# Performance work log

Measured on AMD Instinct MI355X. Metric: run time of the kernel, lower is better.

## Reference

```python
import jax, jax.numpy as jnp
import numpy as np

N = 8000       # n_sample (nodes)
F = 128        # n_feature
H = 128        # n_hidden
E = 256000     # edges (avg degree 32)
NPOOL = 3
K = 10         # propagation steps (args.k)
NC = 2         # n_class
ALPHA = 0.0    # Propagation(alpha=0.0)
CENTS = [400, 20, 1]   # node_pool = round(N**(1/NPOOL)) = 20; n_cent = round(prev/20)


def setup_inputs():
    key = jax.random.key(0)
    ks = jax.random.split(key, 40)
    def nrm(i, shape, scale=1.0):
        return jax.random.normal(ks[i], shape, jnp.float32) * scale
    x = nrm(0, (N, F))
    x_cov = nrm(1, (N, F))
    edge_rows = jax.random.randint(ks[2], (E,), 0, N, dtype=jnp.int32)
    edge_cols = jax.random.randint(ks[3], (E,), 0, N, dtype=jnp.int32)
    adj_vals = jax.random.uniform(ks[4], (E,), jnp.float32)
    raw = jax.random.uniform(ks[5], (E,), jnp.float32) + 0.1
    deg = jax.ops.segment_sum(raw, edge_rows, num_segments=N)
    norm_vals = raw / deg[edge_rows]   # row-normalized adjacency values
    inp = dict(x=x, x_cov=x_cov, edge_rows=edge_rows, edge_cols=edge_cols,
               adj_vals=adj_vals, norm_vals=norm_vals,
               bn_gamma=jnp.ones((F,), jnp.float32), bn_beta=jnp.zeros((F,), jnp.float32))
    i = 6
    for p, nc in enumerate(CENTS):
        inp['c%d_W1' % p] = nrm(i, (F, H), F ** -0.5); i += 1
        inp['c%d_b1' % p] = jnp.zeros((H,), jnp.float32)
        inp['c%d_W2' % p] = nrm(i, (H, nc), H ** -0.5); i += 1
        inp['c%d_b2' % p] = jnp.zeros((nc,), jnp.float32)
    inp['mW1'] = nrm(i, (F, H), F ** -0.5); i += 1
    inp['mb1'] = jnp.zeros((H,), jnp.float32)
    inp['a1'] = jnp.full((1,), 0.25, jnp.float32)   # PReLU slope
    inp['mW2'] = nrm(i, (H, H), H ** -0.5); i += 1
    inp['mb2'] = jnp.zeros((H,), jnp.float32)
    inp['a2'] = jnp.full((1,), 0.25, jnp.float32)
    inp['mW3'] = nrm(i, (H, NC), H ** -0.5); i += 1
    inp['mb3'] = jnp.zeros((NC,), jnp.float32)
    return inp


def _node_corr(z):
    # per-node decomposition of torch.corrcoef(z.T).sum(1):
    #   _node_corr(z).sum(0) == corrcoef(z.T).sum(1)
    zc = z - z.mean(0, keepdims=True)
    zc = zc / (jnp.linalg.norm(zc, axis=0, keepdims=True) + 1e-12)
    return zc * zc.sum(1, keepdims=True)   # [n, F]


def reference(x, x_cov, edge_rows, edge_cols, adj_vals, norm_vals, bn_gamma, bn_beta,
              c0_W1, c0_b1, c0_W2, c0_b2, c1_W1, c1_b1, c1_W2, c1_b2,
              c2_W1, c2_b1, c2_W2, c2_b2, mW1, mb1, a1, mW2, mb2, a2, mW3, mb3):
    # BatchNorm1d (training statistics, biased variance, eps=1e-5)
    mu, var = x.mean(0), x.var(0)
    x = (x - mu) / jnp.sqrt(var + 1e-5) * bn_gamma + bn_beta
    x0 = x

    # --- multi-level clustering / pooling (ClusteringLayer) ---
    cl_params = [(c0_W1, c0_b1, c0_W2, c0_b2), (c1_W1, c1_b1, c1_W2, c1_b2),
                 (c2_W1, c2_b1, c2_W2, c2_b2)]
    masks, corrs = [], []
    xc = x_cov
    for W1, b1, W2, b2 in cl_params:
        h = jax.nn.relu(xc @ W1 + b1)
        S = jax.nn.softmax(h @ W2 + b2, axis=-1)        # soft assignment [n_prev, n_cent]
        corrs.append(_node_corr(xc))                     # corr at the input level
        masks.append(S)
        xc = (S.T @ xc) / (S.sum(0)[:, None] + 1e-12)    # pooled centroid features
    corrs.append(_node_corr(x).sum(0))   # == torch.corrcoef(x.T).sum(1), shape [F]

    # --- gains: sigmoid(corr_{i+1} - normalize_adj(mask_i).T @ corr_i) ---
    gains = []
    for i in range(NPOOL):
        rn = masks[i] / (masks[i].sum(1, keepdims=True) + 1e-12)  # row-normalized (symmetric=False)
        gains.append(jax.nn.sigmoid(corrs[i + 1] - rn.T @ corrs[i]))

    # --- per-feature diagonal-masked sparse matmul chains, restricted to adj's edge set ---
    # projector to original nodes: P_i = masks[0] @ ... @ masks[i]
    P = [masks[0]]
    for i in range(1, NPOOL - 1):
        P.append(P[-1] @ masks[i])
    # (M M^T)[r,c] with M = P_i @ diag(g[:,j]) evaluated only on adj edges, all features at once
    def edge_mask(Pi, g):
        return jnp.einsum('ek,ek,kf->ef', Pi[edge_rows], Pi[edge_cols], g * g)  # [E, F]
    ms = [edge_mask(P[i], gains[i]) for i in reversed(range(NPOOL - 1))]  # i = NPOOL-2 .. 0
    ms = jnp.stack(ms, axis=0).transpose(2, 0, 1)   # [F, NPOOL-1, E]

    def per_feature(a, m_steps):   # sequential carry of adj over feature loop (matches torch)
        def inner(ai, mrow):
            ai = ai * mrow          # adj = adj * mask (elementwise on edge values)
            return ai, ai
        a, temps = jax.lax.scan(inner, a, m_steps)
        return a, temps.sum(0)      # adjs[j] = torch.sparse.sum(stack(temp), dim=0)
    _, adjs = jax.lax.scan(per_feature, adj_vals, ms)   # [F, E] edge values

    # --- diffusion propagation: x <- (1-alpha) * norm_adj @ x + alpha * x0, k times ---
    for _ in range(K):
        agg = jax.ops.segment_sum(norm_vals[:, None] * x[edge_cols], edge_rows, num_segments=N)
        x = (1.0 - ALPHA) * agg + ALPHA * x0

    # --- 3-layer MLP with PReLU + log_softmax ---
    prelu = lambda z, a: jnp.where(z >= 0, z, a * z)
    h = prelu(x @ mW1 + mb1, a1)
    h = prelu(h @ mW2 + mb2, a2)
    logits = h @ mW3 + mb3
    return jax.nn.log_softmax(logits, axis=1), adjs
```

## Files before the change

### kernel.cpp

```cpp
#include <hip/hip_runtime.h>
#include <hip/hip_bf16.h>

typedef __hip_bfloat16 bf16;
typedef __attribute__((ext_vector_type(8))) short s16x8;
typedef __attribute__((ext_vector_type(4))) float f32x4;

static constexpr int NN = 8000;
static constexpr int FF = 128;
static constexpr int EE = 256000;
static constexpr int NC0 = 400;
static constexpr int NC1 = 20;

__device__ __forceinline__ float b2f(bf16 v) { return __bfloat162float(v); }
__device__ __forceinline__ bf16 f2b(float v) { return __float2bfloat16(v); }
__device__ __forceinline__ short f2bs(float v) {
    bf16 h = __float2bfloat16(v);
    return __builtin_bit_cast(short, h);
}
__device__ __forceinline__ float ldw(float v) { return v; }
__device__ __forceinline__ float ldw(bf16 v) { return __bfloat162float(v); }

template <int NW>
__device__ __forceinline__ float block_sum(float v, float* sb) {
    #pragma unroll
    for (int o = 32; o > 0; o >>= 1) v += __shfl_down(v, o, 64);
    int t = threadIdx.x;
    if ((t & 63) == 0) sb[t >> 6] = v;
    __syncthreads();
    float s = 0.f;
    #pragma unroll
    for (int i = 0; i < NW; ++i) s += sb[i];
    __syncthreads();
    return s;
}

template <int NW>
__device__ __forceinline__ float block_max(float v, float* sb) {
    #pragma unroll
    for (int o = 32; o > 0; o >>= 1) v = fmaxf(v, __shfl_down(v, o, 64));
    int t = threadIdx.x;
    if ((t & 63) == 0) sb[t >> 6] = v;
    __syncthreads();
    float m = sb[0];
    #pragma unroll
    for (int i = 1; i < NW; ++i) m = fmaxf(m, sb[i]);
    __syncthreads();
    return m;
}

__global__ void k_fill_b16(bf16* __restrict__ p, float v, long n) {
    long i = (long)blockIdx.x * 256 + threadIdx.x;
    long stride = (long)gridDim.x * 256;
    for (; i < n; i += stride) p[i] = f2b(v);
}

__global__ __launch_bounds__(256)
void k_tsplit(const float* __restrict__ src, bf16* __restrict__ dh, bf16* __restrict__ dl,
              bf16* __restrict__ sh, bf16* __restrict__ sl, int M, int N) {
    __shared__ float t[32][33];
    int bx = blockIdx.x * 32, by = blockIdx.y * 32;
    int x = threadIdx.x;
    for (int y = threadIdx.y; y < 32; y += 8) {
        int m = by + y, n = bx + x;
        if (m < M && n < N) {
            float v = src[(long)m * N + n];
            t[y][x] = v;
            if (sh) {
                bf16 h = f2b(v);
                sh[(long)m * N + n] = h;
                sl[(long)m * N + n] = f2b(v - b2f(h));
            }
        }
    }
    __syncthreads();
    for (int y = threadIdx.y; y < 32; y += 8) {
        int n = bx + y, m = by + x;
        if (n < N && m < M) {
            float v = t[x][y];
            bf16 h = f2b(v);
            dh[(long)n * M + m] = h;
            dl[(long)n * M + m] = f2b(v - b2f(h));
        }
    }
}

__global__ __launch_bounds__(256)
void k_cstat(const float* __restrict__ x, const float* __restrict__ xcov,
             float* __restrict__ acc4) {
    __shared__ float sb[4][256];
    int t = threadIdx.x;
    int col = t & 127, half = t >> 7;
    int rend = min(NN, (blockIdx.x + 1) * 80);
    float sx = 0.f, qx = 0.f, sc = 0.f, qc = 0.f;
    for (int r = blockIdx.x * 80 + half; r < rend; r += 2) {
        float v = x[(long)r * FF + col];
        sx += v; qx += v * v;
        float w = xcov[(long)r * FF + col];
        sc += w; qc += w * w;
    }
    sb[0][t] = sx; sb[1][t] = qx; sb[2][t] = sc; sb[3][t] = qc;
    __syncthreads();
    if (t < 128) {
        atomicAdd(&acc4[0 * 128 + col], sb[0][t] + sb[0][t + 128]);
        atomicAdd(&acc4[1 * 128 + col], sb[1][t] + sb[1][t + 128]);
        atomicAdd(&acc4[2 * 128 + col], sb[2][t] + sb[2][t + 128]);
        atomicAdd(&acc4[3 * 128 + col], sb[3][t] + sb[3][t + 128]);
    }
}

__global__ void k_cfin(const float* __restrict__ acc4, const float* __restrict__ gamma,
                       const float* __restrict__ beta, float* __restrict__ bnsc,
                       float* __restrict__ bnsh, float* __restrict__ statmu,
                       float* __restrict__ statin) {
    int f = threadIdx.x;
    float s = acc4[f], q = acc4[128 + f];
    float mu = s / NN;
    float var = q / NN - mu * mu;
    if (var < 0.f) var = 0.f;
    float rstd = 1.f / sqrtf(var + 1e-5f);
    float sc = gamma[f] * rstd;
    bnsc[f] = sc;
    bnsh[f] = beta[f] - mu * sc;
    float s2 = acc4[256 + f], q2 = acc4[384 + f];
    float m2 = s2 / NN;
    float ss = q2 - s2 * m2;
    if (ss < 0.f) ss = 0.f;
    statmu[f] = m2;
    statin[f] = 1.f / (sqrtf(ss) + 1e-12f);
}

__global__ __launch_bounds__(128)
void k_nodecorr(const float* __restrict__ src, const float* __restrict__ mu,
                const float* __restrict__ invn, float* __restrict__ out) {
    __shared__ float sb[2];
    int n = blockIdx.x, t = threadIdx.x;
    float z = (src[n * FF + t] - mu[t]) * invn[t];
    float tot = block_sum<2>(z, sb);
    out[n * FF + t] = z * tot;
}

__global__ __launch_bounds__(256)
void k_softmax(float* __restrict__ p, int N) {
    __shared__ float sb[4];
    float* row = p + (long)blockIdx.x * N;
    int t = threadIdx.x;
    float m = -1e30f;
    for (int i = t; i < N; i += 256) m = fmaxf(m, row[i]);
    m = block_max<4>(m, sb);
    float s = 0.f;
    for (int i = t; i < N; i += 256) { float e = expf(row[i] - m); row[i] = e; s += e; }
    s = block_sum<4>(s, sb);
    float inv = 1.f / s;
    for (int i = t; i < N; i += 256) row[i] *= inv;
}

__global__ __launch_bounds__(256)
void k_softmax_b16(const float* __restrict__ src, bf16* __restrict__ dst, int N) {
    __shared__ float sb[4];
    const float* row = src + (long)blockIdx.x * N;
    bf16* orow = dst + (long)blockIdx.x * N;
    int t = threadIdx.x;
    float v0 = (t < N) ? row[t] : -1e30f;
    float v1 = (256 + t < N) ? row[256 + t] : -1e30f;
    float m = block_max<4>(fmaxf(v0, v1), sb);
    float e0 = (t < N) ? expf(v0 - m) : 0.f;
    float e1 = (256 + t < N) ? expf(v1 - m) : 0.f;
    float s = block_sum<4>(e0 + e1, sb);
    float inv = 1.f / s;
    if (t < N) orow[t] = f2b(e0 * inv);
    if (256 + t < N) orow[256 + t] = f2b(e1 * inv);
}

template <typename T>
__global__ __launch_bounds__(256)
void k_transpose(const T* __restrict__ src, T* __restrict__ dst, float* __restrict__ cs,
                 int M, int N) {
    __shared__ T t[32][33];
    __shared__ float cbuf[8][33];
    int bx = blockIdx.x * 32, by = blockIdx.y * 32;
    int x = threadIdx.x;
    for (int y = threadIdx.y; y < 32; y += 8) {
        int m = by + y, n = bx + x;
        if (m < M && n < N) t[y][x] = src[(long)m * N + n];
    }
    __syncthreads();
    for (int y = threadIdx.y; y < 32; y += 8) {
        int n = bx + y, m = by + x;
        if (n < N && m < M) dst[(long)n * M + m] = t[x][y];
    }
    if (cs) {
        int ty = threadIdx.y;
        int n = bx + x;
        float p = 0.f;
        if (n < N) {
            for (int y = ty; y < 32; y += 8)
                if (by + y < M) p += ldw(t[y][x]);
        }
        cbuf[ty][x] = p;
        __syncthreads();
        if (ty == 0 && n < N) {
            float s = 0.f;
            #pragma unroll
            for (int i = 0; i < 8; ++i) s += cbuf[i][x];
            atomicAdd(&cs[n], s);
        }
    }
}

__global__ __launch_bounds__(256)
void k_gain0a(const float* __restrict__ T0, const float* __restrict__ cs0,
              float* __restrict__ xc1, float* __restrict__ mu, float* __restrict__ invn) {
    __shared__ float sb[4];
    int f = blockIdx.x;
    float s = 0.f, q = 0.f;
    for (int r = threadIdx.x; r < NC0; r += 256) {
        float v = T0[r * 128 + f] / (cs0[r] + 1e-12f);
        xc1[r * 128 + f] = v;
        s += v; q += v * v;
    }
    s = block_sum<4>(s, sb);
    q = block_sum<4>(q, sb);
    if (threadIdx.x == 0) {
        float m = s / NC0;
        float ss = q - s * m;
        if (ss < 0.f) ss = 0.f;
        mu[f] = m;
        invn[f] = 1.f / (sqrtf(ss) + 1e-12f);
    }
}

__global__ __launch_bounds__(128)
void k_gain0b(const float* __restrict__ xc1, const float* __restrict__ mu,
              const float* __restrict__ invn, const float* __restrict__ T1,
              float* __restrict__ corr1, bf16* __restrict__ g0swz) {
    __shared__ float sb[2];
    int k = blockIdx.x, f = threadIdx.x;
    int ch = k >> 5, rem = k & 31, lhi = rem >> 3, ii = rem & 7;
    int idx = (((ch * 8) + (f >> 4)) * 64 + (lhi * 16 + (f & 15))) * 8 + ii;
    if (k >= NC0) { g0swz[idx] = f2b(0.f); return; }
    float z = (xc1[k * 128 + f] - mu[f]) * invn[f];
    float tot = block_sum<2>(z, sb);
    float corr = z * tot;
    corr1[k * 128 + f] = corr;
    float d = corr - T1[k * 128 + f];
    float g = 1.f / (1.f + expf(-d));
    g0swz[idx] = f2b(g * g);
}

__global__ __launch_bounds__(256)
void k_gain1(const float* __restrict__ T2, const float* __restrict__ cs1,
             const float* __restrict__ T3, bf16* __restrict__ g1swz) {
    __shared__ float xs[20][128];
    __shared__ float mu[128], invn[128];
    __shared__ float sb[4];
    int t = threadIdx.x;
    for (int i = t; i < 20 * 128; i += 256) {
        int r = i >> 7;
        xs[r][i & 127] = T2[i] / (cs1[r] + 1e-12f);
    }
    __syncthreads();
    if (t < 128) {
        float s = 0.f, q = 0.f;
        for (int r = 0; r < 20; ++r) { float v = xs[r][t]; s += v; q += v * v; }
        float m = s / 20.f;
        float ss = q - s * m;
        if (ss < 0.f) ss = 0.f;
        mu[t] = m;
        invn[t] = 1.f / (sqrtf(ss) + 1e-12f);
    }
    __syncthreads();
    for (int r = 0; r < 20; ++r) {
        float z = 0.f;
        if (t < 128) z = (xs[r][t] - mu[t]) * invn[t];
        float tot = block_sum<4>(z, sb);
        if (t < 128) {
            float corr = z * tot;
            float d = corr - T3[r * 128 + t];
            float g = 1.f / (1.f + expf(-d));
            int lhi = (r >> 3) & 3, ii = r & 7;
            g1swz[(((t >> 4) * 64) + (lhi * 16 + (t & 15))) * 8 + ii] = f2b(g * g);
        }
    }
    for (int i = t; i < 12 * 128; i += 256) {
        int k = 20 + (i >> 7), f = i & 127;
        int lhi = (k >> 3) & 3, ii = k & 7;
        g1swz[(((f >> 4) * 64) + (lhi * 16 + (f & 15))) * 8 + ii] = f2b(0.f);
    }
}

template <typename AT, typename WT>
__global__ __launch_bounds__(256)
void k_gemm(const AT* __restrict__ A, const WT* __restrict__ W,
            const float* __restrict__ bias, const float* __restrict__ slope,
            float* __restrict__ C, int M, int K, int N, int act) {
    __shared__ float As[16][68];
    __shared__ float Ws[16][68];
    int tid = threadIdx.x;
    int tx = tid & 15, ty = tid >> 4;
    int m0 = blockIdx.x * 64, n0 = blockIdx.y * 64;
    int KS = gridDim.z;
    int kchunk = ((K + KS * 16 - 1) / (KS * 16)) * 16;
    int kbeg = blockIdx.z * kchunk;
    int kend = min(K, kbeg + kchunk);
    float acc[4][4] = {};
    for (int k0 = kbeg; k0 < kend; k0 += 16) {
        __syncthreads();
        for (int idx = tid; idx < 1024; idx += 256) {
            int r = idx >> 4, kk = idx & 15;
            int m = m0 + r, k = k0 + kk;
            As[kk][r] = (m < M && k < kend) ? ldw(A[(long)m * K + k]) : 0.f;
        }
        for (int idx = tid; idx < 1024; idx += 256) {
            int kk = idx >> 6, n = idx & 63;
            int k = k0 + kk, nn = n0 + n;
            float wv = 0.f;
            if (k < kend && nn < N) wv = ldw(W[(long)k * N + nn]);
            Ws[kk][n] = wv;
        }
        __syncthreads();
        #pragma unroll
        for (int kk = 0; kk < 16; ++kk) {
            float4 a4 = *(const float4*)&As[kk][ty * 4];
            float4 b4 = *(const float4*)&Ws[kk][tx * 4];
            float av[4] = {a4.x, a4.y, a4.z, a4.w};
            float bv[4] = {b4.x, b4.y, b4.z, b4.w};
            #pragma unroll
            for (int i = 0; i < 4; ++i)
                #pragma unroll
                for (int j = 0; j < 4; ++j) acc[i][j] += av[i] * bv[j];
        }
    }
    if (KS > 1) {
        #pragma unroll
        for (int i = 0; i < 4; ++i) {
            int m = m0 + ty * 4 + i;
            if (m >= M) continue;
            #pragma unroll
            for (int j = 0; j < 4; ++j) {
                int n = n0 + tx * 4 + j;
                if (n >= N) continue;
                atomicAdd(&C[(long)m * N + n], acc[i][j]);
            }
        }
    } else {
        float sl = slope ? slope[0] : 0.f;
        #pragma unroll
        for (int i = 0; i < 4; ++i) {
            int m = m0 + ty * 4 + i;
            if (m >= M) continue;
            #pragma unroll
            for (int j = 0; j < 4; ++j) {
                int n = n0 + tx * 4 + j;
                if (n >= N) continue;
                float v = acc[i][j] + (bias ? bias[n] : 0.f);
                if (act == 1) v = fmaxf(v, 0.f);
                else if (act == 2) v = (v >= 0.f) ? v : sl * v;
                C[(long)m * N + n] = v;
            }
        }
    }
}

__global__ __launch_bounds__(256)
void k_gemm2f(const float* __restrict__ A, const float* __restrict__ W1,
              const float* __restrict__ W2, float* __restrict__ C1,
              float* __restrict__ C2, int M, int K, int N) {
    __shared__ float As[16][68];
    __shared__ float Ws1[16][68];
    __shared__ float Ws2[16][68];
    int tid = threadIdx.x;
    int tx = tid & 15, ty = tid >> 4;
    int m0 = blockIdx.x * 64, n0 = blockIdx.y * 64;
    int KS = gridDim.z;
    int kchunk = ((K + KS * 16 - 1) / (KS * 16)) * 16;
    int kbeg = blockIdx.z * kchunk;
    int kend = min(K, kbeg + kchunk);
    float acc1[4][4] = {}, acc2[4][4] = {};
    for (int k0 = kbeg; k0 < kend; k0 += 16) {
        __syncthreads();
        for (int idx = tid; idx < 1024; idx += 256) {
            int r = idx >> 4, kk = idx & 15;
            int m = m0 + r, k = k0 + kk;
            As[kk][r] = (m < M && k < kend) ? A[(long)m * K + k] : 0.f;
        }
        for (int idx = tid; idx < 1024; idx += 256) {
            int kk = idx >> 6, n = idx & 63;
            int k = k0 + kk, nn = n0 + n;
            float w1 = 0.f, w2 = 0.f;
            if (k < kend && nn < N) {
                w1 = W1[(long)k * N + nn];
                w2 = W2[(long)k * N + nn];
            }
            Ws1[kk][n] = w1;
            Ws2[kk][n] = w2;
        }
        __syncthreads();
        #pragma unroll
        for (int kk = 0; kk < 16; ++kk) {
            float4 a4 = *(const float4*)&As[kk][ty * 4];
            float4 b4 = *(const float4*)&Ws1[kk][tx * 4];
            float4 c4 = *(const float4*)&Ws2[kk][tx * 4];
            float av[4] = {a4.x, a4.y, a4.z, a4.w};
            float bv[4] = {b4.x, b4.y, b4.z, b4.w};
            float cv[4] = {c4.x, c4.y, c4.z, c4.w};
            #pragma unroll
            for (int i = 0; i < 4; ++i)
                #pragma unroll
                for (int j = 0; j < 4; ++j) {
                    acc1[i][j] += av[i] * bv[j];
                    acc2[i][j] += av[i] * cv[j];
                }
        }
    }
    #pragma unroll
    for (int i = 0; i < 4; ++i) {
        int m = m0 + ty * 4 + i;
        if (m >= M) continue;
        #pragma unroll
        for (int j = 0; j < 4; ++j) {
            int n = n0 + tx * 4 + j;
            if (n >= N) continue;
            if (KS > 1) {
                atomicAdd(&C1[(long)m * N + n], acc1[i][j]);
                atomicAdd(&C2[(long)m * N + n], acc2[i][j]);
            } else {
                C1[(long)m * N + n] = acc1[i][j];
                C2[(long)m * N + n] = acc2[i][j];
            }
        }
    }
}

template <int PARTS>
__global__ __launch_bounds__(256)
void k_gmm(const bf16* __restrict__ Ah, const bf16* __restrict__ Al,
           const bf16* __restrict__ BTh, const bf16* __restrict__ BTl,
           const float* __restrict__ bias, const float* __restrict__ slope,
           float* __restrict__ C, bf16* __restrict__ Csh, bf16* __restrict__ Csl,
           int padN, int M, int K, int N, int act) {
    __shared__ __align__(16) short At[2][64 * 40];
    __shared__ __align__(16) short Bt[2][64 * 40];
    int tid = threadIdx.x;
    int m0 = blockIdx.x * 64, n0 = blockIdx.y * 64;
    int KS = gridDim.z;
    int kchunk = ((K + KS * 32 - 1) / (KS * 32)) * 32;
    int kbeg = blockIdx.z * kchunk;
    int kend = min(K, kbeg + kchunk);
    int r = tid >> 2, s = tid & 3;
    int l = tid & 63, w = tid >> 6;
    int c = l & 15, g = l >> 4;
    bool arow_ok = (m0 + r < M);
    bool brow_ok = (n0 + r < N);
    const short* ahp = (const short*)Ah + (long)(m0 + r) * K;
    const short* alp = (PARTS >= 3) ? (const short*)Al + (long)(m0 + r) * K : nullptr;
    const short* bhp = (const short*)BTh + (long)(n0 + r) * K;
    const short* blp = (PARTS >= 2) ? (const short*)BTl + (long)(n0 + r) * K : nullptr;
    short* aw = &At[0][r * 40 + 8 * s];
    short* bw = &Bt[0][r * 40 + 8 * s];
    const int afo = (16 * w + c) * 40 + 8 * g;
    f32x4 acc[4] = {};
    for (int k0 = kbeg; k0 < kend; k0 += 32) {
        __syncthreads();
        {
            int kk = k0 + 8 * s;
            bool kok = kk < kend;
            s16x8 av = {}, bv = {};
            if (arow_ok && kok) av = *(const s16x8*)(ahp + kk);
            if (brow_ok && kok) bv = *(const s16x8*)(bhp + kk);
            *(s16x8*)aw = av;
            *(s16x8*)bw = bv;
            if (PARTS >= 2) {
                s16x8 b2 = {};
                if (brow_ok && kok) b2 = *(const s16x8*)(blp + kk);
                *(s16x8*)(bw + 64 * 40) = b2;
            }
            if (PARTS >= 3) {
                s16x8 a2 = {};
                if (arow_ok && kok) a2 = *(const s16x8*)(alp + kk);
                *(s16x8*)(aw + 64 * 40) = a2;
            }
        }
        __syncthreads();
        s16x8 ah_ = *(const s16x8*)&At[0][afo];
        s16x8 al_;
        if (PARTS >= 3) al_ = *(const s16x8*)&At[1][afo];
        #pragma unroll
        for (int nt = 0; nt < 4; ++nt) {
            int bfo = (16 * nt + c) * 40 + 8 * g;
            s16x8 bh_ = *(const s16x8*)&Bt[0][bfo];
            acc[nt] = __builtin_amdgcn_mfma_f32_16x16x32_bf16(ah_, bh_, acc[nt], 0, 0, 0);
            if (PARTS >= 2) {
                s16x8 bl_ = *(const s16x8*)&Bt[1][bfo];
                acc[nt] = __builtin_amdgcn_mfma_f32_16x16x32_bf16(ah_, bl_, acc[nt], 0, 0, 0);
            }
            if (PARTS >= 3)
                acc[nt] = __builtin_amdgcn_mfma_f32_16x16x32_bf16(al_, bh_, acc[nt], 0, 0, 0);
        }
    }
    if (KS > 1) {
        #pragma unroll
        for (int nt = 0; nt < 4; ++nt) {
            int n = n0 + 16 * nt + c;
            if (n >= N) continue;
            #pragma unroll
            for (int q = 0; q < 4; ++q) {
                int m = m0 + 16 * w + 4 * g + q;
                if (m < M) atomicAdd(&C[(long)m * N + n], acc[nt][q]);
            }
        }
    } else if (Csh && Csl) {
        float sl = slope ? slope[0] : 0.f;
        #pragma unroll
        for (int nt = 0; nt < 4; ++nt) {
            int n = n0 + 16 * nt + c;
            if (n >= N) continue;
            float bv = bias ? bias[n] : 0.f;
            #pragma unroll
            for (int q = 0; q < 4; ++q) {
                int m = m0 + 16 * w + 4 * g + q;
                if (m >= M) continue;
                float v = acc[nt][q] + bv;
                if (act == 1) v = fmaxf(v, 0.f);
                else if (act == 2) v = (v >= 0.f) ? v : sl * v;
                bf16 hi = f2b(v);
                Csh[(long)m * N + n] = hi;
                Csl[(long)m * N + n] = f2b(v - b2f(hi));
            }
        }
    } else if (Csh) {
        #pragma unroll
        for (int nt = 0; nt < 4; ++nt) {
            int n = n0 + 16 * nt + c;
            if (n >= padN) continue;
            float bv = (bias && n < N) ? bias[n] : 0.f;
            #pragma unroll
            for (int q = 0; q < 4; ++q) {
                int m = m0 + 16 * w + 4 * g + q;
                if (m >= M) continue;
                float v = (n < N) ? acc[nt][q] + bv : 0.f;
                Csh[(long)m * padN + n] = f2b(v);
            }
        }
    } else {
        float sl = slope ? slope[0] : 0.f;
        #pragma unroll
        for (int nt = 0; nt < 4; ++nt) {
            int n = n0 + 16 * nt + c;
            if (n >= N) continue;
            float bv = bias ? bias[n] : 0.f;
            #pragma unroll
            for (int q = 0; q < 4; ++q) {
                int m = m0 + 16 * w + 4 * g + q;
                if (m >= M) continue;
                float v = acc[nt][q] + bv;
                if (act == 1) v = fmaxf(v, 0.f);
                else if (act == 2) v = (v >= 0.f) ? v : sl * v;
                C[(long)m * N + n] = v;
            }
        }
    }
}

__global__ __launch_bounds__(256)
void k_gmm2(const bf16* __restrict__ Ah,
            const bf16* __restrict__ B1h, const bf16* __restrict__ B1l,
            const bf16* __restrict__ B2h, const bf16* __restrict__ B2l,
            float* __restrict__ C1, float* __restrict__ C2, int M, int K, int N) {
    __shared__ __align__(16) short At[64 * 40];
    __shared__ __align__(16) short Bt[4][64 * 40];
    int tid = threadIdx.x;
    int m0 = blockIdx.x * 64, n0 = blockIdx.y * 64;
    int KS = gridDim.z;
    int kchunk = ((K + KS * 32 - 1) / (KS * 32)) * 32;
    int kbeg = blockIdx.z * kchunk;
    int kend = min(K, kbeg + kchunk);
    int r = tid >> 2, s = tid & 3;
    int l = tid & 63, w = tid >> 6;
    int c = l & 15, g = l >> 4;
    bool arow_ok = (m0 + r < M);
    bool brow_ok = (n0 + r < N);
    const short* ahp = (const short*)Ah + (long)(m0 + r) * K;
    const short* b1hp = (const short*)B1h + (long)(n0 + r) * K;
    const short* b1lp = (const short*)B1l + (long)(n0 + r) * K;
    const short* b2hp = (const short*)B2h + (long)(n0 + r) * K;
    const short* b2lp = (const short*)B2l + (long)(n0 + r) * K;
    short* aw = &At[r * 40 + 8 * s];
    short* bw = &Bt[0][r * 40 + 8 * s];
    const int afo = (16 * w + c) * 40 + 8 * g;
    f32x4 acc1[4] = {}, acc2[4] = {};
    for (int k0 = kbeg; k0 < kend; k0 += 32) {
        __syncthreads();
        {
            int kk = k0 + 8 * s;
            bool kok = kk < kend;
            s16x8 av = {}, v0 = {}, v1 = {}, v2 = {}, v3 = {};
            if (arow_ok && kok) av = *(const s16x8*)(ahp + kk);
            if (brow_ok && kok) {
                v0 = *(const s16x8*)(b1hp + kk);
                v1 = *(const s16x8*)(b1lp + kk);
                v2 = *(const s16x8*)(b2hp + kk);
                v3 = *(const s16x8*)(b2lp + kk);
            }
            *(s16x8*)aw = av;
            *(s16x8*)(bw + 0 * 2560) = v0;
            *(s16x8*)(bw + 1 * 2560) = v1;
            *(s16x8*)(bw + 2 * 2560) = v2;
            *(s16x8*)(bw + 3 * 2560) = v3;
        }
        __syncthreads();
        s16x8 a_ = *(const s16x8*)&At[afo];
        #pragma unroll
        for (int nt = 0; nt < 4; ++nt) {
            int bfo = (16 * nt + c) * 40 + 8 * g;
            s16x8 b1h_ = *(const s16x8*)&Bt[0][bfo];
            s16x8 b1l_ = *(const s16x8*)&Bt[1][bfo];
            s16x8 b2h_ = *(const s16x8*)&Bt[2][bfo];
            s16x8 b2l_ = *(const s16x8*)&Bt[3][bfo];
            acc1[nt] = __builtin_amdgcn_mfma_f32_16x16x32_bf16(a_, b1h_, acc1[nt], 0, 0, 0);
            acc1[nt] = __builtin_amdgcn_mfma_f32_16x16x32_bf16(a_, b1l_, acc1[nt], 0, 0, 0);
            acc2[nt] = __builtin_amdgcn_mfma_f32_16x16x32_bf16(a_, b2h_, acc2[nt], 0, 0, 0);
            acc2[nt] = __builtin_amdgcn_mfma_f32_16x16x32_bf16(a_, b2l_, acc2[nt], 0, 0, 0);
        }
    }
    #pragma unroll
    for (int nt = 0; nt < 4; ++nt) {
        int n = n0 + 16 * nt + c;
        if (n >= N) continue;
        #pragma unroll
        for (int q = 0; q < 4; ++q) {
            int m = m0 + 16 * w + 4 * g + q;
            if (m >= M) continue;
            if (KS > 1) {
                atomicAdd(&C1[(long)m * N + n], acc1[nt][q]);
                atomicAdd(&C2[(long)m * N + n], acc2[nt][q]);
            } else {
                C1[(long)m * N + n] = acc1[nt][q];
                C2[(long)m * N + n] = acc2[nt][q];
            }
        }
    }
}

__global__ __launch_bounds__(256)
void k_edge(const int* __restrict__ er, const int* __restrict__ ec,
            const float* __restrict__ adj,
            const bf16* __restrict__ S0b, const bf16* __restrict__ P1hp,
            const bf16* __restrict__ g0swz, const bf16* __restrict__ g1swz,
            bf16* __restrict__ outp, int E) {
    __shared__ __align__(16) short Ot[128 * 72];
    const int tid = threadIdx.x;
    const int e0 = blockIdx.x * 64;
    const int l = tid & 63, w = tid >> 6;
    const int c = l & 15, g = l >> 4;
    const int eb = 16 * w + (l >> 2), seg = l & 3;
    const int rn = er[e0 + eb], cn = ec[e0 + eb];
    const short* S0s = (const short*)S0b;
    const short* rrow = S0s + (long)rn * 400 + 8 * seg;
    const short* crow = S0s + (long)cn * 400 + 8 * seg;
    const int pa = ((((l & 15) << 2) + g) << 2);
    const s16x8* g0p = (const s16x8*)g0swz;
    f32x4 acc0[8] = {};
    f32x4 acc1[8] = {};
    s16x8 ar = *(const s16x8*)(rrow);
    s16x8 ac = *(const s16x8*)(crow);
    #pragma unroll 1
    for (int ch = 0; ch < 13; ++ch) {
        s16x8 nar, nac;
        if (ch < 12) {
            nar = *(const s16x8*)(rrow + 32 * (ch + 1));
            nac = *(const s16x8*)(crow + 32 * (ch + 1));
        }
        s16x8 wv;
        #pragma unroll
        for (int i = 0; i < 8; ++i) {
            float av = __uint_as_float(((unsigned)(unsigned short)ar[i]) << 16);
            float bv = __uint_as_float(((unsigned)(unsigned short)ac[i]) << 16);
            wv[i] = f2bs(av * bv);
        }
        int4 wvi = __builtin_bit_cast(int4, wv);
        int4 wfi;
        wfi.x = __builtin_amdgcn_ds_bpermute(pa, wvi.x);
        wfi.y = __builtin_amdgcn_ds_bpermute(pa, wvi.y);
        wfi.z = __builtin_amdgcn_ds_bpermute(pa, wvi.z);
        wfi.w = __builtin_amdgcn_ds_bpermute(pa, wvi.w);
        s16x8 wfrag = __builtin_bit_cast(s16x8, wfi);
        const s16x8* gc = g0p + (long)ch * 512 + l;
        #pragma unroll
        for (int t = 0; t < 8; ++t)
            acc0[t] = __builtin_amdgcn_mfma_f32_16x16x32_bf16(gc[t * 64], wfrag, acc0[t], 0, 0, 0);
        ar = nar; ac = nac;
    }
    {
        s16x8 wv = {};
        if (seg < 3) {
            const short* P1s = (const short*)P1hp;
            s16x8 pr = *(const s16x8*)(P1s + (long)rn * 24 + 8 * seg);
            s16x8 pc = *(const s16x8*)(P1s + (long)cn * 24 + 8 * seg);
            #pragma unroll
            for (int i = 0; i < 8; ++i) {
                float av = __uint_as_float(((unsigned)(unsigned short)pr[i]) << 16);
                float bv = __uint_as_float(((unsigned)(unsigned short)pc[i]) << 16);
                wv[i] = f2bs(av * bv);
            }
        }
        int4 wvi = __builtin_bit_cast(int4, wv);
        int4 wfi;
        wfi.x = __builtin_amdgcn_ds_bpermute(pa, wvi.x);
        wfi.y = __builtin_amdgcn_ds_bpermute(pa, wvi.y);
        wfi.z = __builtin_amdgcn_ds_bpermute(pa, wvi.z);
        wfi.w = __builtin_amdgcn_ds_bpermute(pa, wvi.w);
        s16x8 wfrag = __builtin_bit_cast(s16x8, wfi);
        const s16x8* g1p = (const s16x8*)g1swz;
        #pragma unroll
        for (int t = 0; t < 8; ++t)
            acc1[t] = __builtin_amdgcn_mfma_f32_16x16x32_bf16(g1p[t * 64 + l], wfrag, acc1[t], 0, 0, 0);
    }
    const int ecl = 16 * w + c;
    float pre = adj[e0 + ecl];
    #pragma unroll
    for (int t = 0; t < 8; ++t) {
        float m10 = acc0[t][0], m11 = acc0[t][1], m12 = acc0[t][2], m13 = acc0[t][3];
        float m00 = acc1[t][0], m01 = acc1[t][1], m02 = acc1[t][2], m03 = acc1[t][3];
        float q0 = m00 * m10, q1 = m01 * m11, q2 = m02 * m12, q3 = m03 * m13;
        float eq1 = q0, eq2 = q0 * q1, eq3 = eq2 * q2;
        float incg = eq3 * q3;
        float u = __shfl_up(incg, 16, 64); if (g >= 1) incg *= u;
        u = __shfl_up(incg, 32, 64); if (g >= 2) incg *= u;
        float exg = __shfl_up(incg, 16, 64); if (g == 0) exg = 1.f;
        float tot = __shfl(incg, 48 + c, 64);
        float base = pre * exg;
        pre *= tot;
        int fb = 16 * t + 4 * g;
        Ot[(fb + 0) * 72 + ecl] = f2bs(base * m00 * (1.f + m10));
        Ot[(fb + 1) * 72 + ecl] = f2bs(base * eq1 * m01 * (1.f + m11));
        Ot[(fb + 2) * 72 + ecl] = f2bs(base * eq2 * m02 * (1.f + m12));
        Ot[(fb + 3) * 72 + ecl] = f2bs(base * eq3 * m03 * (1.f + m13));
    }
    __syncthreads();
    const int fo = tid & 127, hf = tid >> 7;
    if (fo < 127 || e0 < 240000) {
        const short* lsrc = &Ot[fo * 72 + hf * 32];
        short* gdst = (short*)outp + (long)fo * E + e0 + hf * 32;
        #pragma unroll
        for (int q = 0; q < 4; ++q)
            *(s16x8*)(gdst + 8 * q) = *(const s16x8*)(lsrc + 8 * q);
    }
}

__global__ void k_count(const int* __restrict__ er, int* __restrict__ counts, int E) {
    int e = blockIdx.x * 256 + threadIdx.x;
    if (e < E) atomicAdd(&counts[er[e]], 1);
}

__global__ __launch_bounds__(256)
void k_scan(const int* __restrict__ counts, int* __restrict__ rs,
            int* __restrict__ cur, int R) {
    __shared__ int buf[2][256];
    int t = threadIdx.x;
    const int PER = 32;
    int b = t * PER;
    int s = 0;
    for (int i = 0; i < PER; ++i) {
        int idx = b + i;
        if (idx < R) s += counts[idx];
    }
    buf[0][t] = s;
    __syncthreads();
    int src = 0;
    for (int off = 1; off < 256; off <<= 1) {
        int v = buf[src][t];
        if (t >= off) v += buf[src][t - off];
        buf[1 - src][t] = v;
        __syncthreads();
        src = 1 - src;
    }
    int base = (t > 0) ? buf[src][t - 1] : 0;
    for (int i = 0; i < PER; ++i) {
        int idx = b + i;
        if (idx < R) {
            int c = counts[idx];
            rs[idx] = base;
            cur[idx] = base;
            base += c;
        }
    }
    if (t == 255) rs[R] = buf[src][255];
}

__global__ void k_scatter(const int* __restrict__ er, const int* __restrict__ ec,
                          const float* __restrict__ nv, int* __restrict__ cur,
                          int2* __restrict__ cpack, int E) {
    int e = blockIdx.x * 256 + threadIdx.x;
    if (e < E) {
        int r = er[e];
        int p = atomicAdd(&cur[r], 1);
        cpack[p] = make_int2(ec[e], __float_as_int(nv[e]));
    }
}

__global__ __launch_bounds__(256)
void k_spmv4(const int* __restrict__ rs, const int2* __restrict__ cpack,
             const float* __restrict__ xin, float* __restrict__ xout,
             const float* __restrict__ sc4, const float* __restrict__ sh4, int R) {
    int lane = threadIdx.x & 31;
    int r = blockIdx.x * 8 + (threadIdx.x >> 5);
    if (r >= R) return;
    int jb = rs[r], je = rs[r + 1];
    float4 acc = {0.f, 0.f, 0.f, 0.f};
    if (sc4) {
        float4 sc = ((const float4*)sc4)[lane];
        float4 sh = ((const float4*)sh4)[lane];
        int j = jb;
        for (; j + 4 <= je; j += 4) {
            int2 cv0 = cpack[j], cv1 = cpack[j + 1], cv2 = cpack[j + 2], cv3 = cpack[j + 3];
            float4 x0 = ((const float4*)(xin + (long)cv0.x * FF))[lane];
            float4 x1 = ((const float4*)(xin + (long)cv1.x * FF))[lane];
            float4 x2 = ((const float4*)(xin + (long)cv2.x * FF))[lane];
            float4 x3 = ((const float4*)(xin + (long)cv3.x * FF))[lane];
            float v0 = __int_as_float(cv0.y), v1 = __int_as_float(cv1.y);
            float v2 = __int_as_float(cv2.y), v3 = __int_as_float(cv3.y);
            acc.x += v0 * (x0.x * sc.x + sh.x) + v1 * (x1.x * sc.x + sh.x)
                   + v2 * (x2.x * sc.x + sh.x) + v3 * (x3.x * sc.x + sh.x);
            acc.y += v0 * (x0.y * sc.y + sh.y) + v1 * (x1.y * sc.y + sh.y)
                   + v2 * (x2.y * sc.y + sh.y) + v3 * (x3.y * sc.y + sh.y);
            acc.z += v0 * (x0.z * sc.z + sh.z) + v1 * (x1.z * sc.z + sh.z)
                   + v2 * (x2.z * sc.z + sh.z) + v3 * (x3.z * sc.z + sh.z);
            acc.w += v0 * (x0.w * sc.w + sh.w) + v1 * (x1.w * sc.w + sh.w)
                   + v2 * (x2.w * sc.w + sh.w) + v3 * (x3.w * sc.w + sh.w);
        }
        for (; j < je; ++j) {
            int2 cv = cpack[j];
            float v = __int_as_float(cv.y);
            float4 xv = ((const float4*)(xin + (long)cv.x * FF))[lane];
            acc.x += v * (xv.x * sc.x + sh.x);
            acc.y += v * (xv.y * sc.y + sh.y);
            acc.z += v * (xv.z * sc.z + sh.z);
            acc.w += v * (xv.w * sc.w + sh.w);
        }
    } else {
        int j = jb;
        for (; j + 4 <= je; j += 4) {
            int2 cv0 = cpack[j], cv1 = cpack[j + 1], cv2 = cpack[j + 2], cv3 = cpack[j + 3];
            float4 x0 = ((const float4*)(xin + (long)cv0.x * FF))[lane];
            float4 x1 = ((const float4*)(xin + (long)cv1.x * FF))[lane];
            float4 x2 = ((const float4*)(xin + (long)cv2.x * FF))[lane];
            float4 x3 = ((const float4*)(xin + (long)cv3.x * FF))[lane];
            float v0 = __int_as_float(cv0.y), v1 = __int_as_float(cv1.y);
            float v2 = __int_as_float(cv2.y), v3 = __int_as_float(cv3.y);
            acc.x += v0 * x0.x; acc.y += v0 * x0.y; acc.z += v0 * x0.z; acc.w += v0 * x0.w;
            acc.x += v1 * x1.x; acc.y += v1 * x1.y; acc.z += v1 * x1.z; acc.w += v1 * x1.w;
            acc.x += v2 * x2.x; acc.y += v2 * x2.y; acc.z += v2 * x2.z; acc.w += v2 * x2.w;
            acc.x += v3 * x3.x; acc.y += v3 * x3.y; acc.z += v3 * x3.z; acc.w += v3 * x3.w;
        }
        for (; j < je; ++j) {
            int2 cv = cpack[j];
            float v = __int_as_float(cv.y);
            float4 xv = ((const float4*)(xin + (long)cv.x * FF))[lane];
            acc.x += v * xv.x; acc.y += v * xv.y; acc.z += v * xv.z; acc.w += v * xv.w;
        }
    }
    ((float4*)(xout + (long)r * FF))[lane] = acc;
}

__global__ __launch_bounds__(256)
void k_fc128(const float* __restrict__ xin, const float* __restrict__ W,
             const float* __restrict__ b, const float* __restrict__ a,
             float* __restrict__ hout, int nblk) {
    __shared__ float Ws[16384];
    __shared__ float xs[2][128];
    int t = threadIdx.x;
    for (int i = t; i < 16384; i += 256) Ws[i] = W[i];
    float slope = a[0];
    int half = t >> 7, tt = t & 127;
    float bb = b[tt];
    __syncthreads();
    for (int n = blockIdx.x * 2 + half; n < NN; n += nblk * 2) {
        xs[half][tt] = xin[(long)n * FF + tt];
        __syncthreads();
        float a0 = 0.f, a1 = 0.f, a2 = 0.f, a3 = 0.f;
        #pragma unroll 8
        for (int k = 0; k < 128; k += 4) {
            a0 += xs[half][k + 0] * Ws[(k + 0) * 128 + tt];
            a1 += xs[half][k + 1] * Ws[(k + 1) * 128 + tt];
            a2 += xs[half][k + 2] * Ws[(k + 2) * 128 + tt];
            a3 += xs[half][k + 3] * Ws[(k + 3) * 128 + tt];
        }
        float acc = bb + ((a0 + a1) + (a2 + a3));
        hout[(long)n * FF + tt] = (acc >= 0.f) ? acc : slope * acc;
        __syncthreads();
    }
}

__global__ __launch_bounds__(256)
void k_mlp_tail(const float* __restrict__ hin, const float* __restrict__ W2,
                const float* __restrict__ b2, const float* __restrict__ a2,
                const float* __restrict__ W3, const float* __restrict__ b3,
                bf16* __restrict__ outA, bf16* __restrict__ outB, int nblk) {
    __shared__ float Ws[16384];
    __shared__ float xs[2][128];
    __shared__ float red[8];
    int t = threadIdx.x;
    for (int i = t; i < 16384; i += 256) Ws[i] = W2[i];
    float slope = a2[0];
    int half = t >> 7, tt = t & 127;
    float bb = b2[tt];
    float w30 = W3[tt * 2 + 0], w31 = W3[tt * 2 + 1];
    float b30 = b3[0], b31 = b3[1];
    __syncthreads();
    for (int n = blockIdx.x * 2 + half; n < NN; n += nblk * 2) {
        xs[half][tt] = hin[(long)n * FF + tt];
        __syncthreads();
        float a0 = 0.f, a1 = 0.f, a2_ = 0.f, a3 = 0.f;
        #pragma unroll 8
        for (int k = 0; k < 128; k += 4) {
            a0 += xs[half][k + 0] * Ws[(k + 0) * 128 + tt];
            a1 += xs[half][k + 1] * Ws[(k + 1) * 128 + tt];
            a2_ += xs[half][k + 2] * Ws[(k + 2) * 128 + tt];
            a3 += xs[half][k + 3] * Ws[(k + 3) * 128 + tt];
        }
        float acc = bb + ((a0 + a1) + (a2_ + a3));
        float h2 = (acc >= 0.f) ? acc : slope * acc;
        float l0 = h2 * w30, l1 = h2 * w31;
        #pragma unroll
        for (int o = 32; o > 0; o >>= 1) {
            l0 += __shfl_down(l0, o, 64);
            l1 += __shfl_down(l1, o, 64);
        }
        int wid = t >> 6;
        if ((t & 63) == 0) { red[wid] = l0; red[4 + wid] = l1; }
        __syncthreads();
        if (tt == 0) {
            float L0 = red[half * 2] + red[half * 2 + 1] + b30;
            float L1 = red[4 + half * 2] + red[4 + half * 2 + 1] + b31;
            float m = fmaxf(L0, L1);
            float lse = m + logf(expf(L0 - m) + expf(L1 - m));
            bf16 v0 = f2b(L0 - lse), v1 = f2b(L1 - lse);
            outA[n * 2 + 0] = v0; outA[n * 2 + 1] = v1;
            outB[n * 2 + 0] = v0; outB[n * 2 + 1] = v1;
        }
        __syncthreads();
    }
}

extern "C" void kernel_launch(void* const* d_in, const int* in_sizes, int n_in,
                              void* d_out, int out_size, void* d_ws, size_t ws_size,
                              hipStream_t stream) {
    const float* x     = (const float*)d_in[0];
    const float* xcov  = (const float*)d_in[1];
    const int*   erow  = (const int*)d_in[2];
    const int*   ecol  = (const int*)d_in[3];
    const float* adjv  = (const float*)d_in[4];
    const float* normv = (const float*)d_in[5];
    const float* gamma = (const float*)d_in[6];
    const float* beta  = (const float*)d_in[7];
    const float* c0W1 = (const float*)d_in[8];  const float* c0b1 = (const float*)d_in[9];
    const float* c0W2 = (const float*)d_in[10]; const float* c0b2 = (const float*)d_in[11];
    const float* c1W1 = (const float*)d_in[12]; const float* c1b1 = (const float*)d_in[13];
    const float* c1W2 = (const float*)d_in[14]; const float* c1b2 = (const float*)d_in[15];
    const float* mW1 = (const float*)d_in[20]; const float* mb1 = (const float*)d_in[21];
    const float* a1  = (const float*)d_in[22];
    const float* mW2 = (const float*)d_in[23]; const float* mb2 = (const float*)d_in[24];
    const float* a2  = (const float*)d_in[25];
    const float* mW3 = (const float*)d_in[26]; const float* mb3 = (const float*)d_in[27];

    char* B = (char*)d_out;
    bf16* logitsA = (bf16*)B;
    bf16* logitsB = (bf16*)(B + 32000);
    bf16* adjsOut = (bf16*)(B + 64000);

    auto ovl = [](const void* a, size_t an, const void* b, size_t bn) {
        const char* A = (const char*)a; const char* Bp = (const char*)b;
        return (A < Bp + bn) && (Bp < A + an);
    };
    size_t outBytes = (size_t)out_size * 2;
    static const int expSize[28] = {1024000,1024000,256000,256000,256000,256000,128,128,
                                    16384,128,51200,400, 16384,128,2560,20, 16384,128,128,1,
                                    16384,128,1, 16384,128,1, 256,2};
    int code = 0;
    if (n_in != 28) code = 200;
    else for (int i = 0; i < 28 && !code; ++i) if (in_sizes[i] != expSize[i]) code = 200;
    if (!code && ovl(d_ws, ws_size, d_out, outBytes)) code = 300;
    if (!code) {
        for (int i = 0; i < 28; ++i) {
            size_t bytes = (size_t)in_sizes[i] * 4;
            if (ovl(d_ws, ws_size, d_in[i], bytes)) { code = 400; break; }
            if (ovl(d_out, outBytes, d_in[i], bytes)) { code = 500; break; }
        }
    }
    if (!code && ws_size < (size_t)6935040) code = 600;
    if (code) {
        k_fill_b16<<<64, 256, 0, stream>>>(logitsA, (float)code, 16000);
        k_fill_b16<<<64, 256, 0, stream>>>(logitsB, (float)code, 16000);
        k_fill_b16<<<2048, 256, 0, stream>>>(adjsOut, 0.0f, (outBytes - 64000) / 2);
        return;
    }

    char* ws = (char*)d_ws;
    bf16*  S0b   = (bf16*)(ws + 0);
    bf16*  P1hp  = (bf16*)(ws + 6400000);
    bf16*  g0swz = (bf16*)(ws + 6784000);
    bf16*  g1swz = (bf16*)(ws + 6890496);

    char* S = B + 64000;
    float* xbn   = (float*)(S + 0);
    float* ping  = (float*)(S + 4096000);
    float* h0    = (float*)(S + 8192000);
    float* hh2   = (float*)(S + 12288000);
    float* S0f   = (float*)(S + 16384000);
    bf16*  S0Tb  = (bf16*)(S + 29184000);
    int*   rs    = (int*)(S + 36224000);
    int*   cur   = (int*)(S + 36256016);
    int2*  cpack = (int2*)(S + 36288016);
    float* T0    = (float*)(S + 38400512);
    float* T1    = (float*)(S + 38605312);
    float* xc1   = (float*)(S + 38810112);
    float* corr1 = (float*)(S + 39014912);
    float* h1    = (float*)(S + 39219712);
    float* S1    = (float*)(S + 39424512);
    float* S1T   = (float*)(S + 39456512);
    float* T2    = (float*)(S + 39488512);
    float* T3    = (float*)(S + 39498752);
    float* cs0   = (float*)(S + 39529472);
    float* cs1   = (float*)(S + 39531072);
    float* bnsc  = (float*)(S + 39532032);
    float* bnsh  = (float*)(S + 39532544);
    float* statmu= (float*)(S + 39533056);
    float* statin= (float*)(S + 39533568);
    float* acc4  = (float*)(S + 39534080);
    bf16* xcovh  = (bf16*)(S + 39749120);
    bf16* xcovl  = (bf16*)(S + 41797120);
    bf16* xcovTh = (bf16*)(S + 43845120);
    bf16* xcovTl = (bf16*)(S + 45893120);
    bf16* hh2Th  = (bf16*)(S + 47941120);
    bf16* hh2Tl  = (bf16*)(S + 49989120);
    bf16* h0h    = (bf16*)(S + 52037120);
    bf16* h0l    = (bf16*)(S + 54085120);
    bf16* W1Th   = (bf16*)(S + 56133120);
    bf16* W1Tl   = (bf16*)(S + 56165888);
    bf16* W2Th   = (bf16*)(S + 56198656);
    bf16* W2Tl   = (bf16*)(S + 56301056);
    bf16* S1Th   = (bf16*)(S + 56403456);
    bf16* S1Tl   = (bf16*)(S + 56419456);

    hipMemsetAsync(acc4, 0, 4 * 128 * 4, stream);
    k_cstat<<<100, 256, 0, stream>>>(x, xcov, acc4);
    k_cfin<<<1, 128, 0, stream>>>(acc4, gamma, beta, bnsc, bnsh, statmu, statin);
    k_nodecorr<<<NN, 128, 0, stream>>>(xcov, statmu, statin, hh2);
    k_tsplit<<<dim3(4, 250), dim3(32, 8), 0, stream>>>(xcov, xcovTh, xcovTl, xcovh, xcovl, NN, FF);
    k_tsplit<<<dim3(4, 250), dim3(32, 8), 0, stream>>>(hh2, hh2Th, hh2Tl, nullptr, nullptr, NN, FF);
    k_tsplit<<<dim3(4, 4), dim3(32, 8), 0, stream>>>(c0W1, W1Th, W1Tl, nullptr, nullptr, 128, 128);
    k_tsplit<<<dim3(13, 4), dim3(32, 8), 0, stream>>>(c0W2, W2Th, W2Tl, nullptr, nullptr, 128, NC0);
    k_gmm<3><<<dim3(125, 2, 1), 256, 0, stream>>>(xcovh, xcovl, W1Th, W1Tl, c0b1, nullptr,
                                                  nullptr, h0h, h0l, 0, NN, 128, 128, 1);
    k_gmm<3><<<dim3(125, 7, 1), 256, 0, stream>>>(h0h, h0l, W2Th, W2Tl, c0b2, nullptr,
                                                  S0f, nullptr, nullptr, 0, NN, 128, NC0, 0);
    k_softmax_b16<<<NN, 256, 0, stream>>>(S0f, S0b, NC0);
    hipMemsetAsync(cs0, 0, NC0 * 4, stream);
    k_transpose<bf16><<<dim3(13, 250), dim3(32, 8), 0, stream>>>(S0b, S0Tb, cs0, NN, NC0);
    hipMemsetAsync(T0, 0, NC0 * 128 * 4, stream);
    hipMemsetAsync(T1, 0, NC0 * 128 * 4, stream);
    k_gmm2<<<dim3(7, 2, 16), 256, 0, stream>>>(S0Tb, xcovTh, xcovTl, hh2Th, hh2Tl,
                                               T0, T1, NC0, NN, 128);
    k_gain0a<<<128, 256, 0, stream>>>(T0, cs0, xc1, statmu, statin);
    k_gain0b<<<416, 128, 0, stream>>>(xc1, statmu, statin, T1, corr1, g0swz);
    k_gemm<float, float><<<dim3(7, 2, 1), 256, 0, stream>>>(xc1, c1W1, c1b1, nullptr, h1, NC0, 128, 128, 1);
    k_gemm<float, float><<<dim3(7, 1, 1), 256, 0, stream>>>(h1, c1W2, c1b2, nullptr, S1, NC0, 128, NC1, 0);
    k_softmax<<<NC0, 256, 0, stream>>>(S1, NC1);
    hipMemsetAsync(cs1, 0, NC1 * 4, stream);
    k_transpose<float><<<dim3(1, 13), dim3(32, 8), 0, stream>>>(S1, S1T, cs1, NC0, NC1);
    k_tsplit<<<dim3(1, 13), dim3(32, 8), 0, stream>>>(S1, S1Th, S1Tl, nullptr, nullptr, NC0, NC1);
    hipMemsetAsync(T2, 0, NC1 * 128 * 4, stream);
    hipMemsetAsync(T3, 0, NC1 * 128 * 4, stream);
    k_gemm2f<<<dim3(1, 2, 4), 256, 0, stream>>>(S1T, xc1, corr1, T2, T3, NC1, NC0, 128);
    k_gain1<<<1, 256, 0, stream>>>(T2, cs1, T3, g1swz);
    k_gmm<2><<<dim3(125, 1, 1), 256, 0, stream>>>(S0b, nullptr, S1Th, S1Tl, nullptr, nullptr,
                                                  nullptr, P1hp, nullptr, 24, NN, NC0, NC1, 0);
    hipMemsetAsync(cur, 0, NN * 4, stream);
    k_count<<<1000, 256, 0, stream>>>(erow, cur, EE);
    k_scan<<<1, 256, 0, stream>>>(cur, rs, cur, NN);
    k_scatter<<<1000, 256, 0, stream>>>(erow, ecol, normv, cur, cpack, EE);
    k_spmv4<<<1000, 256, 0, stream>>>(rs, cpack, x, xbn, bnsc, bnsh, NN);
    float* xa = xbn;
    float* xb = ping;
    for (int it = 1; it < 10; ++it) {
        k_spmv4<<<1000, 256, 0, stream>>>(rs, cpack, xa, xb, nullptr, nullptr, NN);
        float* t = xa; xa = xb; xb = t;
    }
    k_fc128<<<250, 256, 0, stream>>>(ping, mW1, mb1, a1, h0, 250);
    k_mlp_tail<<<250, 256, 0, stream>>>(h0, mW2, mb2, a2, mW3, mb3, logitsA, logitsB, 250);
    k_edge<<<EE / 64, 256, 0, stream>>>(erow, ecol, adjv, S0b, P1hp, g0swz, g1swz, adjsOut, EE);
}
```

Before: 766.4 us.

## Move MLP layers to split-bf16 MFMA GEMMs and defer acc1 in edge kernel

Replaces the scalar fp32 shared-memory MLP kernels with hi/lo bf16 splits of activations and weights fed into the existing k_gmm<3> MFMA GEMM path, plus a small wave-per-node head kernel for the final projection and log-softmax. In the edge kernel, the single-step g1 MFMA accumulator is now computed per tile inside the epilogue instead of being held across the main loop, which lowers register pressure. The trade-off is extra split/transpose launches and buffer reuse of workspace arrays (hh2Th, xcovh), which assumes those buffers are free at that point.

New measurement: 737.0 us. 3.8% less time.

```diff
diff --git a/kernel.cpp b/kernel.cpp
--- a/kernel.cpp
+++ b/kernel.cpp
@@ -52,6 +52,17 @@
     long i = (long)blockIdx.x * 256 + threadIdx.x;
     long stride = (long)gridDim.x * 256;
     for (; i < n; i += stride) p[i] = f2b(v);
+}
+
+__global__ void k_split(const float* __restrict__ src, bf16* __restrict__ dh,
+                        bf16* __restrict__ dl, int n) {
+    int i = blockIdx.x * 256 + threadIdx.x;
+    if (i < n) {
+        float v = src[i];
+        bf16 h = f2b(v);
+        dh[i] = h;
+        dl[i] = f2b(v - b2f(h));
+    }
 }
 
 __global__ __launch_bounds__(256)
@@ -659,37 +670,7 @@
     const short* crow = S0s + (long)cn * 400 + 8 * seg;
     const int pa = ((((l & 15) << 2) + g) << 2);
     const s16x8* g0p = (const s16x8*)g0swz;
-    f32x4 acc0[8] = {};
-    f32x4 acc1[8] = {};
-    s16x8 ar = *(const s16x8*)(rrow);
-    s16x8 ac = *(const s16x8*)(crow);
-    #pragma unroll 1
-    for (int ch = 0; ch < 13; ++ch) {
-        s16x8 nar, nac;
-        if (ch < 12) {
-            nar = *(const s16x8*)(rrow + 32 * (ch + 1));
-            nac = *(const s16x8*)(crow + 32 * (ch + 1));
-        }
-        s16x8 wv;
-        #pragma unroll
-        for (int i = 0; i < 8; ++i) {
-            float av = __uint_as_float(((unsigned)(unsigned short)ar[i]) << 16);
-            float bv = __uint_as_float(((unsigned)(unsigned short)ac[i]) << 16);
-            wv[i] = f2bs(av * bv);
-        }
-        int4 wvi = __builtin_bit_cast(int4, wv);
-        int4 wfi;
-        wfi.x = __builtin_amdgcn_ds_bpermute(pa, wvi.x);
-        wfi.y = __builtin_amdgcn_ds_bpermute(pa, wvi.y);
-        wfi.z = __builtin_amdgcn_ds_bpermute(pa, wvi.z);
-        wfi.w = __builtin_amdgcn_ds_bpermute(pa, wvi.w);
-        s16x8 wfrag = __builtin_bit_cast(s16x8, wfi);
-        const s16x8* gc = g0p + (long)ch * 512 + l;
-        #pragma unroll
-        for (int t = 0; t < 8; ++t)
-            acc0[t] = __builtin_amdgcn_mfma_f32_16x16x32_bf16(gc[t * 64], wfrag, acc0[t], 0, 0, 0);
-        ar = nar; ac = nac;
-    }
+    s16x8 wfrag1;
     {
         s16x8 wv = {};
         if (seg < 3) {
@@ -709,18 +690,47 @@
         wfi.y = __builtin_amdgcn_ds_bpermute(pa, wvi.y);
         wfi.z = __builtin_amdgcn_ds_bpermute(pa, wvi.z);
         wfi.w = __builtin_amdgcn_ds_bpermute(pa, wvi.w);
+        wfrag1 = __builtin_bit_cast(s16x8, wfi);
+    }
+    f32x4 acc0[8] = {};
+    s16x8 ar = *(const s16x8*)(rrow);
+    s16x8 ac = *(const s16x8*)(crow);
+    #pragma unroll 1
+    for (int ch = 0; ch < 13; ++ch) {
+        s16x8 nar, nac;
+        if (ch < 12) {
+            nar = *(const s16x8*)(rrow + 32 * (ch + 1));
+            nac = *(const s16x8*)(crow + 32 * (ch + 1));
+        }
+        s16x8 wv;
+        #pragma unroll
+        for (int i = 0; i < 8; ++i) {
+            float av = __uint_as_float(((unsigned)(unsigned short)ar[i]) << 16);
+            float bv = __uint_as_float(((unsigned)(unsigned short)ac[i]) << 16);
+            wv[i] = f2bs(av * bv);
+        }
+        int4 wvi = __builtin_bit_cast(int4, wv);
+        int4 wfi;
+        wfi.x = __builtin_amdgcn_ds_bpermute(pa, wvi.x);
+        wfi.y = __builtin_amdgcn_ds_bpermute(pa, wvi.y);
+        wfi.z = __builtin_amdgcn_ds_bpermute(pa, wvi.z);
+        wfi.w = __builtin_amdgcn_ds_bpermute(pa, wvi.w);
         s16x8 wfrag = __builtin_bit_cast(s16x8, wfi);
-        const s16x8* g1p = (const s16x8*)g1swz;
+        const s16x8* gc = g0p + (long)ch * 512 + l;
         #pragma unroll
         for (int t = 0; t < 8; ++t)
-            acc1[t] = __builtin_amdgcn_mfma_f32_16x16x32_bf16(g1p[t * 64 + l], wfrag, acc1[t], 0, 0, 0);
-    }
+            acc0[t] = __builtin_amdgcn_mfma_f32_16x16x32_bf16(gc[t * 64], wfrag, acc0[t], 0, 0, 0);
+        ar = nar; ac = nac;
+    }
+    const s16x8* g1p = (const s16x8*)g1swz;
     const int ecl = 16 * w + c;
     float pre = adj[e0 + ecl];
     #pragma unroll
     for (int t = 0; t < 8; ++t) {
+        f32x4 z4 = {0.f, 0.f, 0.f, 0.f};
+        f32x4 a1 = __builtin_amdgcn_mfma_f32_16x16x32_bf16(g1p[t * 64 + l], wfrag1, z4, 0, 0, 0);
         float m10 = acc0[t][0], m11 = acc0[t][1], m12 = acc0[t][2], m13 = acc0[t][3];
-        float m00 = acc1[t][0], m01 = acc1[t][1], m02 = acc1[t][2], m03 = acc1[t][3];
+        float m00 = a1[0], m01 = a1[1], m02 = a1[2], m03 = a1[3];
         float q0 = m00 * m10, q1 = m01 * m11, q2 = m02 * m12, q3 = m03 * m13;
         float eq1 = q0, eq2 = q0 * q1, eq3 = eq2 * q2;
         float incg = eq3 * q3;
@@ -863,82 +873,36 @@
 }
 
 __global__ __launch_bounds__(256)
-void k_fc128(const float* __restrict__ xin, const float* __restrict__ W,
-             const float* __restrict__ b, const float* __restrict__ a,
-             float* __restrict__ hout, int nblk) {
-    __shared__ float Ws[16384];
-    __shared__ float xs[2][128];
-    int t = threadIdx.x;
-    for (int i = t; i < 16384; i += 256) Ws[i] = W[i];
-    float slope = a[0];
-    int half = t >> 7, tt = t & 127;
-    float bb = b[tt];
-    __syncthreads();
-    for (int n = blockIdx.x * 2 + half; n < NN; n += nblk * 2) {
-        xs[half][tt] = xin[(long)n * FF + tt];
-        __syncthreads();
-        float a0 = 0.f, a1 = 0.f, a2 = 0.f, a3 = 0.f;
-        #pragma unroll 8
-        for (int k = 0; k < 128; k += 4) {
-            a0 += xs[half][k + 0] * Ws[(k + 0) * 128 + tt];
-            a1 += xs[half][k + 1] * Ws[(k + 1) * 128 + tt];
-            a2 += xs[half][k + 2] * Ws[(k + 2) * 128 + tt];
-            a3 += xs[half][k + 3] * Ws[(k + 3) * 128 + tt];
-        }
-        float acc = bb + ((a0 + a1) + (a2 + a3));
-        hout[(long)n * FF + tt] = (acc >= 0.f) ? acc : slope * acc;
-        __syncthreads();
-    }
-}
-
-__global__ __launch_bounds__(256)
-void k_mlp_tail(const float* __restrict__ hin, const float* __restrict__ W2,
-                const float* __restrict__ b2, const float* __restrict__ a2,
-                const float* __restrict__ W3, const float* __restrict__ b3,
-                bf16* __restrict__ outA, bf16* __restrict__ outB, int nblk) {
-    __shared__ float Ws[16384];
-    __shared__ float xs[2][128];
-    __shared__ float red[8];
-    int t = threadIdx.x;
-    for (int i = t; i < 16384; i += 256) Ws[i] = W2[i];
-    float slope = a2[0];
-    int half = t >> 7, tt = t & 127;
-    float bb = b2[tt];
-    float w30 = W3[tt * 2 + 0], w31 = W3[tt * 2 + 1];
-    float b30 = b3[0], b31 = b3[1];
-    __syncthreads();
-    for (int n = blockIdx.x * 2 + half; n < NN; n += nblk * 2) {
-        xs[half][tt] = hin[(long)n * FF + tt];
-        __syncthreads();
-        float a0 = 0.f, a1 = 0.f, a2_ = 0.f, a3 = 0.f;
-        #pragma unroll 8
-        for (int k = 0; k < 128; k += 4) {
-            a0 += xs[half][k + 0] * Ws[(k + 0) * 128 + tt];
-            a1 += xs[half][k + 1] * Ws[(k + 1) * 128 + tt];
-            a2_ += xs[half][k + 2] * Ws[(k + 2) * 128 + tt];
-            a3 += xs[half][k + 3] * Ws[(k + 3) * 128 + tt];
-        }
-        float acc = bb + ((a0 + a1) + (a2_ + a3));
-        float h2 = (acc >= 0.f) ? acc : slope * acc;
-        float l0 = h2 * w30, l1 = h2 * w31;
-        #pragma unroll
-        for (int o = 32; o > 0; o >>= 1) {
-            l0 += __shfl_down(l0, o, 64);
-            l1 += __shfl_down(l1, o, 64);
-        }
-        int wid = t >> 6;
-        if ((t & 63) == 0) { red[wid] = l0; red[4 + wid] = l1; }
-        __syncthreads();
-        if (tt == 0) {
-            float L0 = red[half * 2] + red[half * 2 + 1] + b30;
-            float L1 = red[4 + half * 2] + red[4 + half * 2 + 1] + b31;
-            float m = fmaxf(L0, L1);
-            float lse = m + logf(expf(L0 - m) + expf(L1 - m));
-            bf16 v0 = f2b(L0 - lse), v1 = f2b(L1 - lse);
-            outA[n * 2 + 0] = v0; outA[n * 2 + 1] = v1;
-            outB[n * 2 + 0] = v0; outB[n * 2 + 1] = v1;
-        }
-        __syncthreads();
+void k_head(const bf16* __restrict__ h2h, const bf16* __restrict__ h2l,
+            const float* __restrict__ W3, const float* __restrict__ b3,
+            bf16* __restrict__ outA, bf16* __restrict__ outB) {
+    int lane = threadIdx.x & 63;
+    int n = blockIdx.x * 4 + (threadIdx.x >> 6);
+    int e0 = 2 * lane;
+    const short* hp = (const short*)h2h + (long)n * FF + e0;
+    const short* lp = (const short*)h2l + (long)n * FF + e0;
+    short2 hv = *(const short2*)hp;
+    short2 lv = *(const short2*)lp;
+    float v0 = __uint_as_float(((unsigned)(unsigned short)hv.x) << 16)
+             + __uint_as_float(((unsigned)(unsigned short)lv.x) << 16);
+    float v1 = __uint_as_float(((unsigned)(unsigned short)hv.y) << 16)
+             + __uint_as_float(((unsigned)(unsigned short)lv.y) << 16);
+    float4 wv = *(const float4*)(W3 + 2 * e0);
+    float l0 = v0 * wv.x + v1 * wv.z;
+    float l1 = v0 * wv.y + v1 * wv.w;
+    #pragma unroll
+    for (int o = 32; o > 0; o >>= 1) {
+        l0 += __shfl_down(l0, o, 64);
+        l1 += __shfl_down(l1, o, 64);
+    }
+    if (lane == 0) {
+        float L0 = l0 + b3[0];
+        float L1 = l1 + b3[1];
+        float m = fmaxf(L0, L1);
+        float lse = m + logf(expf(L0 - m) + expf(L1 - m));
+        bf16 o0 = f2b(L0 - lse), o1 = f2b(L1 - lse);
+        outA[n * 2 + 0] = o0; outA[n * 2 + 1] = o1;
+        outB[n * 2 + 0] = o0; outB[n * 2 + 1] = o1;
     }
 }
 
@@ -1086,7 +1050,15 @@
         k_spmv4<<<1000, 256, 0, stream>>>(rs, cpack, xa, xb, nullptr, nullptr, NN);
         float* t = xa; xa = xb; xb = t;
     }
-    k_fc128<<<250, 256, 0, stream>>>(ping, mW1, mb1, a1, h0, 250);
-    k_mlp_tail<<<250, 256, 0, stream>>>(h0, mW2, mb2, a2, mW3, mb3, logitsA, logitsB, 250);
+    bf16* pingh = hh2Th;
+    bf16* pingl = hh2Tl;
+    k_split<<<4000, 256, 0, stream>>>(xa, pingh, pingl, NN * FF);
+    k_tsplit<<<dim3(4, 4), dim3(32, 8), 0, stream>>>(mW1, W1Th, W1Tl, nullptr, nullptr, 128, 128);
+    k_tsplit<<<dim3(4, 4), dim3(32, 8), 0, stream>>>(mW2, W2Th, W2Tl, nullptr, nullptr, 128, 128);
+    k_gmm<3><<<dim3(125, 2, 1), 256, 0, stream>>>(pingh, pingl, W1Th, W1Tl, mb1, a1,
+                                                  nullptr, h0h, h0l, 0, NN, 128, 128, 2);
+    k_gmm<3><<<dim3(125, 2, 1), 256, 0, stream>>>(h0h, h0l, W2Th, W2Tl, mb2, a2,
+                                                  nullptr, xcovh, xcovl, 0, NN, 128, 128, 2);
+    k_head<<<2000, 256, 0, stream>>>(xcovh, xcovl, mW3, mb3, logitsA, logitsB);
     k_edge<<<EE / 64, 256, 0, stream>>>(erow, ecol, adjv, S0b, P1hp, g0swz, g1swz, adjsOut, EE);
 }
```
